# Performance work log

Hardware: AMD Instinct MI355X
Metric: run time of the kernel (lower is better)

Reference implementation:

```python
import jax, jax.numpy as jnp
import numpy as np

W_WORKERS = 2
Q_LEN = 16
HIDDEN = 4096
N_HEADS = 32
N_KV = 8
HEAD_DIM = 128
L_SHARED = 8192
L_WORKER = 2048
THETA = 10000.0


def rotate_half(x):
    x1, x2 = jnp.split(x, 2, axis=-1)
    return jnp.concatenate((-x2, x1), axis=-1)


def rope_cos_sin(pos):
    # pos: int array [...]; returns cos,sin of shape [..., HEAD_DIM] (HF convention: freqs duplicated)
    inv = 1.0 / (THETA ** (jnp.arange(0, HEAD_DIM, 2, dtype=jnp.float32) / HEAD_DIM))
    ang = pos[..., None].astype(jnp.float32) * inv
    emb = jnp.concatenate((ang, ang), axis=-1)
    return jnp.cos(emb), jnp.sin(emb)


def setup_inputs() -> dict:
    key = jax.random.key(0)
    ks = jax.random.split(key, 16)
    std = 0.02
    # new keys are appended at positions L_WORKER..L_WORKER+Q-1 of each worker's own segment
    pos_new = jnp.broadcast_to(L_WORKER + jnp.arange(Q_LEN), (W_WORKERS, Q_LEN))
    cos_new, sin_new = rope_cos_sin(pos_new)
    return {
        'hidden_states': jax.random.normal(ks[0], (W_WORKERS, Q_LEN, HIDDEN), jnp.float32),
        'Wq': jax.random.normal(ks[1], (N_HEADS * HEAD_DIM, HIDDEN), jnp.float32) * std,
        'bq': jnp.zeros((N_HEADS * HEAD_DIM,), jnp.float32),
        'Wk': jax.random.normal(ks[2], (N_KV * HEAD_DIM, HIDDEN), jnp.float32) * std,
        'bk': jnp.zeros((N_KV * HEAD_DIM,), jnp.float32),
        'Wv': jax.random.normal(ks[3], (N_KV * HEAD_DIM, HIDDEN), jnp.float32) * std,
        'bv': jnp.zeros((N_KV * HEAD_DIM,), jnp.float32),
        'Wo': jax.random.normal(ks[4], (HIDDEN, N_HEADS * HEAD_DIM), jnp.float32) * std,
        'seg_shared_k': jax.random.normal(ks[5], (N_KV, L_SHARED, HEAD_DIM), jnp.float32),
        'seg_shared_v': jax.random.normal(ks[6], (N_KV, L_SHARED, HEAD_DIM), jnp.float32),
        'w0_k': jax.random.normal(ks[7], (N_KV, L_WORKER, HEAD_DIM), jnp.float32),
        'w0_v': jax.random.normal(ks[8], (N_KV, L_WORKER, HEAD_DIM), jnp.float32),
        'w1_k': jax.random.normal(ks[9], (N_KV, L_WORKER, HEAD_DIM), jnp.float32),
        'w1_v': jax.random.normal(ks[10], (N_KV, L_WORKER, HEAD_DIM), jnp.float32),
        'cos_new': cos_new,
        'sin_new': sin_new,
    }


def reference(hidden_states, Wq, bq, Wk, bk, Wv, bv, Wo,
              seg_shared_k, seg_shared_v, w0_k, w0_v, w1_k, w1_v,
              cos_new, sin_new):
    W, Q, _ = hidden_states.shape
    scale = HEAD_DIM ** -0.5
    # projections -> [W, n_heads, Q, D]
    q = (hidden_states @ Wq.T + bq).reshape(W, Q, N_HEADS, HEAD_DIM).transpose(0, 2, 1, 3)
    k_new = (hidden_states @ Wk.T + bk).reshape(W, Q, N_KV, HEAD_DIM).transpose(0, 2, 1, 3)
    v_new = (hidden_states @ Wv.T + bv).reshape(W, Q, N_KV, HEAD_DIM).transpose(0, 2, 1, 3)
    # rope new keys (unsqueeze_dim=1: broadcast over kv heads)
    c, s = cos_new[:, None], sin_new[:, None]
    k_new = k_new * c + rotate_half(k_new) * s
    # cache update: segment 0 = shared prompt, segment 1/2 = worker 0/1 own cache (grows by Q)
    keys = [seg_shared_k,
            jnp.concatenate([w0_k, k_new[0]], axis=1),
            jnp.concatenate([w1_k, k_new[1]], axis=1)]
    values = [seg_shared_v,
              jnp.concatenate([w0_v, v_new[0]], axis=1),
              jnp.concatenate([w1_v, v_new[1]], axis=1)]
    frag_lens = [L_SHARED, L_WORKER + Q, L_WORKER + Q]
    # worker w's view: [shared, other worker's cache, own cache]
    orders = [[0, 2, 1], [0, 1, 2]]
    loc = np.zeros((3, W_WORKERS, Q), dtype=np.int32)
    for w, order in enumerate(orders):
        pos = 0
        for seg in reversed(order):
            pos += frag_lens[seg]
            loc[seg, w] = np.arange(pos - Q, pos)
    loc = jnp.asarray(loc)  # [S, W, Q]
    cos_q, sin_q = rope_cos_sin(loc)  # [S, W, Q, D]
    # hogwild_rope: queries rotated per (segment, worker) location -> [S, W, H, Q, D]
    rq = q[None] * cos_q[:, :, None] + rotate_half(q)[None] * sin_q[:, :, None]
    rep = N_HEADS // N_KV
    scores, v_parts = [], []
    for seg in range(3):
        k_s = jnp.repeat(keys[seg], rep, axis=0)  # GQA expand [H, L_s, D]
        sc = jnp.einsum('whqd,hld->whql', rq[seg], k_s) * scale
        mask = jnp.arange(frag_lens[seg])[None, None, None, :] <= loc[seg][:, None, :, None]
        scores.append(jnp.where(mask, sc, jnp.finfo(sc.dtype).min))
        v_parts.append(jnp.repeat(values[seg], rep, axis=0))
    scores = jnp.concatenate(scores, axis=-1)        # [W, H, Q, Ltot] joint softmax over fragments
    probs = jax.nn.softmax(scores, axis=-1)
    v_all = jnp.concatenate(v_parts, axis=1)         # [H, Ltot, D]
    attn = jnp.einsum('whql,hld->whqd', probs, v_all)
    out = attn.transpose(0, 2, 1, 3).reshape(W, Q, N_HEADS * HEAD_DIM) @ Wo.T
    return out
```

## Files before the change

### kernel.cpp

```cpp
#include <hip/hip_runtime.h>
#include <hip/hip_fp16.h>
#include <cstdint>
#include <cstddef>

#define QL 16
#define LSH 8192
#define LWK 2048
#define SCALE 0.08838834764831845f

typedef __attribute__((ext_vector_type(8))) short short8;
typedef __attribute__((ext_vector_type(4))) short short4v;
typedef __attribute__((ext_vector_type(4))) float f32x4;
typedef __attribute__((ext_vector_type(8))) unsigned short ushort8v;

#if defined(__has_builtin)
#if __has_builtin(__builtin_amdgcn_mfma_f32_16x16x16bf16_1k)
#define HAVE_MFMA16 1
#endif
#endif

__device__ __forceinline__ unsigned short f2bf(float f) {
  unsigned int u = __float_as_uint(f);
  u += 0x7fffu + ((u >> 16) & 1u);
  return (unsigned short)(u >> 16);
}
__device__ __forceinline__ float bf2f(unsigned short b) {
  return __uint_as_float(((unsigned int)b) << 16);
}

__device__ __forceinline__ void gload_lds16(const float* g, float* lds) {
  __builtin_amdgcn_global_load_lds(
      (const __attribute__((address_space(1))) void*)g,
      (__attribute__((address_space(3))) void*)lds, 16, 0, 0);
}

__device__ __forceinline__ void gload_f4(float4& d, const float* p) {
  asm volatile("global_load_dwordx4 %0, %1, off"
               : "=v"(d)
               : "v"((const __attribute__((address_space(1))) float*)p));
}
__device__ __forceinline__ void gload_f1(float& d, const float* p) {
  asm volatile("global_load_dword %0, %1, off"
               : "=v"(d)
               : "v"((const __attribute__((address_space(1))) float*)p));
}
__device__ __forceinline__ void gload_s8(short8& d, const unsigned short* p) {
  asm volatile("global_load_dwordx4 %0, %1, off"
               : "=v"(d)
               : "v"((const __attribute__((address_space(1))) unsigned short*)p));
}

__global__ __launch_bounds__(256) void k_cast(
    const float* __restrict__ in, unsigned short* __restrict__ outp, int n4)
{
  int i = blockIdx.x * 256 + threadIdx.x;
  if (i < n4) {
    float4 v = ((const float4*)in)[i];
    ushort4 p; p.x = f2bf(v.x); p.y = f2bf(v.y); p.z = f2bf(v.z); p.w = f2bf(v.w);
    ((ushort4*)outp)[i] = p;
  }
}

__global__ __launch_bounds__(256) void k_gemm4(
    const unsigned short* __restrict__ Xbf,
    const float* __restrict__ W0, const float* __restrict__ W1, const float* __restrict__ W2,
    const float* __restrict__ b0, const float* __restrict__ b1, const float* __restrict__ b2,
    float* __restrict__ outA, float* __restrict__ outB, int Ntot)
{
  __shared__ float Ws[2][16 * 516];
  const int bx = blockIdx.x;
  const int n0 = (bx >> 1) * 16;
  const int khalf = bx & 1;
  const float* W; const float* bias; int row0;
  if (n0 < 4096)      { W = W0; bias = b0; row0 = n0; }
  else if (n0 < 5120) { W = W1; bias = b1; row0 = n0 - 4096; }
  else                { W = W2; bias = b2; row0 = n0 - 5120; }
  const int t = threadIdx.x;
  const int w_id = t >> 6;
  const int lane = t & 63;
  const int l15 = lane & 15;
  const int quad = lane >> 4;
  const int cb0 = khalf * 2048;
  const int wk = w_id * 128;

  f32x4 C0 = {0.f,0.f,0.f,0.f}, C1 = {0.f,0.f,0.f,0.f};
  short8 xa0[4], xa1[4];

  auto stage = [&](int c, int b) {
    const int cbase = cb0 + c * 512;
#pragma unroll
    for (int i = 0; i < 8; ++i) {
      int idx = w_id * 8 + i;
      int r = idx >> 1, hh = idx & 1;
      const float* g = W + (size_t)(row0 + r) * 4096 + cbase + hh * 256 + lane * 4;
      gload_lds16(g, &Ws[b][r * 516 + hh * 256]);
    }
  };

  stage(0, 0);
#pragma unroll
  for (int c = 0; c < 4; ++c) {
    const int cbase = cb0 + c * 512;
#pragma unroll
    for (int ks = 0; ks < 4; ++ks) {
      int ko = wk + ks * 32 + quad * 8;
      gload_s8(xa0[ks], Xbf + (size_t)l15 * 4096 + cbase + ko);
      gload_s8(xa1[ks], Xbf + (size_t)(16 + l15) * 4096 + cbase + ko);
    }
    __builtin_amdgcn_sched_barrier(0);
    if (c < 3) {
      stage(c + 1, (c + 1) & 1);
      asm volatile("s_waitcnt vmcnt(8)" ::: "memory");
    } else {
      asm volatile("s_waitcnt vmcnt(0)" ::: "memory");
    }
    __builtin_amdgcn_sched_barrier(0);
    __builtin_amdgcn_s_barrier();
    __builtin_amdgcn_sched_barrier(0);
    const float* Wsb = Ws[c & 1];
#pragma unroll
    for (int ks = 0; ks < 4; ++ks) {
      int ko = wk + ks * 32 + quad * 8;
      f32x4 wlo = *(const f32x4*)(&Wsb[l15 * 516 + ko]);
      f32x4 whi = *(const f32x4*)(&Wsb[l15 * 516 + ko + 4]);
      short8 bfr;
      bfr[0] = (short)f2bf(wlo[0]); bfr[1] = (short)f2bf(wlo[1]);
      bfr[2] = (short)f2bf(wlo[2]); bfr[3] = (short)f2bf(wlo[3]);
      bfr[4] = (short)f2bf(whi[0]); bfr[5] = (short)f2bf(whi[1]);
      bfr[6] = (short)f2bf(whi[2]); bfr[7] = (short)f2bf(whi[3]);
      C0 = __builtin_amdgcn_mfma_f32_16x16x32_bf16(xa0[ks], bfr, C0, 0, 0, 0);
      C1 = __builtin_amdgcn_mfma_f32_16x16x32_bf16(xa1[ks], bfr, C1, 0, 0, 0);
    }
    __builtin_amdgcn_sched_barrier(0);
    __builtin_amdgcn_s_barrier();
    __builtin_amdgcn_sched_barrier(0);
  }
  float* Red = &Ws[0][0];
#pragma unroll
  for (int i = 0; i < 4; ++i) {
    Red[w_id * 512 + (quad * 4 + i) * 16 + l15] = C0[i];
    Red[w_id * 512 + 256 + (quad * 4 + i) * 16 + l15] = C1[i];
  }
  __syncthreads();
  float* dst = khalf ? outB : outA;
#pragma unroll
  for (int e = t; e < 512; e += 256) {
    float s = Red[e] + Red[512 + e] + Red[1024 + e] + Red[1536 + e];
    int m = e >> 4, n = e & 15;
    if (khalf == 0 && bias) s += bias[row0 + n];
    dst[(size_t)m * Ntot + n0 + n] = s;
  }
}

__global__ __launch_bounds__(256) void k_add(
    const float* __restrict__ A, const float* __restrict__ B,
    float* __restrict__ o, int n4)
{
  int i = blockIdx.x * 256 + threadIdx.x;
  if (i < n4) {
    float4 a = ((const float4*)A)[i], b = ((const float4*)B)[i];
    float4 r; r.x = a.x + b.x; r.y = a.y + b.y; r.z = a.z + b.z; r.w = a.w + b.w;
    ((float4*)o)[i] = r;
  }
}

__global__ __launch_bounds__(256) void k_rope(
    const float* __restrict__ qA, const float* __restrict__ qB,
    const float* __restrict__ cosn, const float* __restrict__ sinn,
    unsigned short* __restrict__ rq, unsigned short* __restrict__ knew,
    unsigned short* __restrict__ vnew)
{
  const int g = blockIdx.x * 256 + threadIdx.x;
  const float LOGTH = 9.210340371976184f;
  if (g < 393216) {
    int d = g & 127, q = (g >> 7) & 15, head = (g >> 11) & 31, w = (g >> 16) & 1, var = g >> 17;
    int tok = w * 16 + q;
    int col = head * 128 + d;
    size_t ix = (size_t)tok * 6144 + col;
    float val = qA[ix] + qB[ix];
    size_t ir = (d < 64) ? ix + 64 : ix - 64;
    float rot = qA[ir] + qB[ir];
    if (d < 64) rot = -rot;
    int pos = (var == 0 ? 12304 : (var == 1 ? 4112 : 2048)) + q;
    int i = d & 63;
    float inv = expf(-(float)i * (LOGTH / 64.0f));
    float ang = (float)pos * inv;
    float c = cosf(ang), s = sinf(ang);
    rq[g] = f2bf((val * c + rot * s) * SCALE);
  } else {
    int g2 = g - 393216;
    if (g2 < 65536) {
      int isv = (g2 >= 32768);
      if (isv) g2 -= 32768;
      int d = g2 & 127, q = (g2 >> 7) & 15, h = (g2 >> 11) & 7, w = (g2 >> 14) & 1;
      int tok = w * 16 + q;
      if (isv) {
        size_t ix = (size_t)tok * 6144 + 5120 + h * 128 + d;
        vnew[g2] = f2bf(qA[ix] + qB[ix]);
      } else {
        size_t ix = (size_t)tok * 6144 + 4096 + h * 128 + d;
        float val = qA[ix] + qB[ix];
        size_t ir = (d < 64) ? ix + 64 : ix - 64;
        float rot = qA[ir] + qB[ir];
        if (d < 64) rot = -rot;
        float c = cosn[tok * 128 + d], s = sinn[tok * 128 + d];
        knew[g2] = f2bf(val * c + rot * s);
      }
    }
  }
}

__global__ __launch_bounds__(512, 2) void k_attn(
    const float* __restrict__ shk, const float* __restrict__ shv,
    const float* __restrict__ w0k, const float* __restrict__ w0v,
    const float* __restrict__ w1k, const float* __restrict__ w1v,
    const unsigned short* __restrict__ rq,
    const unsigned short* __restrict__ knew, const unsigned short* __restrict__ vnew,
    __half* __restrict__ accP, float* __restrict__ lP)
{
  __shared__ alignas(16) unsigned short Ks[2][64 * 136];
  __shared__ alignas(16) unsigned short Vts[2][128 * 72];
#ifndef HAVE_MFMA16
  __shared__ alignas(16) unsigned short Plds[8 * 16 * 72];
#endif

  const int h = blockIdx.x / 50;
  const int cidx = blockIdx.x % 50;
  int kind, k0, nk; bool is_new;
  if (cidx < 32)      { kind = 0; k0 = cidx * 256; nk = 256; is_new = false; }
  else if (cidx < 41) { int c = cidx - 32; kind = 1; k0 = c * 256; nk = (c == 8) ? 16 : 256; is_new = (c == 8); }
  else                { int c = cidx - 41; kind = 2; k0 = c * 256; nk = (c == 8) ? 16 : 256; is_new = (c == 8); }

  const int t = threadIdx.x;
  const int w_id = t >> 6;
  const int lane = t & 63;
  const int l15 = lane & 15;
  const int quad = lane >> 4;
  const int worker = w_id >> 2;
  const int hq = w_id & 3;
  const int col4 = t & 31;
  const int rowb = t >> 5;
  const int dv = t & 127;
  const int tg = t >> 7;

  int var; bool causal;
  if (kind == 0)      { var = 0; causal = false; }
  else if (kind == 1) { var = (worker == 0) ? 2 : 1; causal = (worker == 0); }
  else                { var = (worker == 1) ? 2 : 1; causal = (worker == 1); }

  const float* Ksrc = (kind == 0) ? (shk + (size_t)h * LSH * 128)
                     : (kind == 1) ? (w0k + (size_t)h * LWK * 128)
                                   : (w1k + (size_t)h * LWK * 128);
  const float* Vsrc = (kind == 0) ? (shv + (size_t)h * LSH * 128)
                     : (kind == 1) ? (w0v + (size_t)h * LWK * 128)
                                   : (w1v + (size_t)h * LWK * 128);
  const int wseg = (kind == 2) ? 1 : 0;
  const unsigned short* knsrc = knew + ((size_t)wseg * 8 + h) * 16 * 128;
  const unsigned short* vnsrc = vnew + ((size_t)wseg * 8 + h) * 16 * 128;

  const int head = h * 4 + hq;
  short8 arq[4];
  {
    const unsigned short* base =
        rq + ((((size_t)var * 2 + worker) * 32 + head) * 16 + l15) * 128 + quad * 8;
#pragma unroll
    for (int ks = 0; ks < 4; ++ks) arq[ks] = *(const short8*)(base + ks * 32);
  }

  float lrow = 0.f;
  f32x4 acc[8];
#pragma unroll
  for (int dt = 0; dt < 8; ++dt) acc[dt] = {0.f,0.f,0.f,0.f};

  float4 kf[4];
  float  vf[16];

  const float* kbase = Ksrc + (size_t)(k0 + rowb) * 128 + col4 * 4;
  const float* vbase = Vsrc + (size_t)(k0 + tg * 8) * 128 + dv;

  auto issue_tile = [&](int st) {
    const float* kp = kbase + (size_t)st * 64 * 128;
#pragma unroll
    for (int i = 0; i < 4; ++i) gload_f4(kf[i], kp + (size_t)i * 16 * 128);
    const float* vp = vbase + (size_t)st * 64 * 128;
#pragma unroll
    for (int g = 0; g < 2; ++g)
#pragma unroll
      for (int i = 0; i < 8; ++i)
        gload_f1(vf[g * 8 + i], vp + (size_t)(g * 32 + i) * 128);
  };

  const int nst = (nk + 63) >> 6;
  if (!is_new) {
    issue_tile(0);
  } else {
#pragma unroll
    for (int i = 0; i < 4; ++i) {
      ushort4 p = *(const ushort4*)(knsrc + (size_t)((i * 16 + rowb) & 15) * 128 + col4 * 4);
      kf[i].x = bf2f(p.x); kf[i].y = bf2f(p.y);
      kf[i].z = bf2f(p.z); kf[i].w = bf2f(p.w);
    }
#pragma unroll
    for (int g = 0; g < 2; ++g)
#pragma unroll
      for (int i = 0; i < 8; ++i)
        vf[g * 8 + i] = bf2f(vnsrc[(size_t)((g * 32 + tg * 8 + i) & 15) * 128 + dv]);
  }

  for (int st = 0; st < nst; ++st) {
    const int pb = st & 1;
    asm volatile("s_waitcnt vmcnt(0)" ::: "memory");
    __builtin_amdgcn_sched_barrier(0);
#pragma unroll
    for (int i = 0; i < 4; ++i) {
      ushort4 p; p.x = f2bf(kf[i].x); p.y = f2bf(kf[i].y);
      p.z = f2bf(kf[i].z); p.w = f2bf(kf[i].w);
      *(ushort4*)(&Ks[pb][(i * 16 + rowb) * 136 + col4 * 4]) = p;
    }
#pragma unroll
    for (int g = 0; g < 2; ++g) {
      ushort8v p;
#pragma unroll
      for (int i = 0; i < 8; ++i) p[i] = f2bf(vf[g * 8 + i]);
      *(ushort8v*)(&Vts[pb][dv * 72 + (g * 4 + tg) * 8]) = p;
    }
    if (st + 1 < nst) issue_tile(st + 1);
    asm volatile("s_waitcnt lgkmcnt(0)" ::: "memory");
    __builtin_amdgcn_sched_barrier(0);
    __builtin_amdgcn_s_barrier();
    __builtin_amdgcn_sched_barrier(0);

    f32x4 S[4];
#pragma unroll
    for (int nt = 0; nt < 4; ++nt) S[nt] = {0.f,0.f,0.f,0.f};
#pragma unroll
    for (int ks = 0; ks < 4; ++ks)
#pragma unroll
      for (int nt = 0; nt < 4; ++nt) {
        short8 kfr = *(const short8*)(&Ks[pb][(nt * 16 + l15) * 136 + ks * 32 + quad * 8]);
        S[nt] = __builtin_amdgcn_mfma_f32_16x16x32_bf16(kfr, arq[ks], S[nt], 0, 0, 0);
      }
    if (is_new) {
#pragma unroll
      for (int nt = 0; nt < 4; ++nt)
#pragma unroll
        for (int i = 0; i < 4; ++i) {
          int loc = st * 64 + nt * 16 + quad * 4 + i;
          if (loc >= nk || (causal && loc > l15)) S[nt][i] = -3.0e38f;
        }
    }
    float rs = 0.0f;
#pragma unroll
    for (int nt = 0; nt < 4; ++nt)
#pragma unroll
      for (int i = 0; i < 4; ++i) {
        float p = __expf(fminf(S[nt][i], 60.0f));
        S[nt][i] = p;
        rs += p;
      }
#ifdef HAVE_MFMA16
    short4v pv[4];
#pragma unroll
    for (int nt = 0; nt < 4; ++nt) {
      short4v pp;
      pp[0] = (short)f2bf(S[nt][0]); pp[1] = (short)f2bf(S[nt][1]);
      pp[2] = (short)f2bf(S[nt][2]); pp[3] = (short)f2bf(S[nt][3]);
      pv[nt] = pp;
    }
#else
#pragma unroll
    for (int nt = 0; nt < 4; ++nt)
#pragma unroll
      for (int i = 0; i < 4; ++i)
        Plds[w_id * (16 * 72) + l15 * 72 + nt * 16 + quad * 4 + i] = f2bf(S[nt][i]);
#endif
    rs += __shfl_xor(rs, 16, 64);
    rs += __shfl_xor(rs, 32, 64);
    lrow += rs;

#ifdef HAVE_MFMA16
#pragma unroll
    for (int dt = 0; dt < 8; ++dt)
#pragma unroll
      for (int kc = 0; kc < 4; ++kc) {
        short4v vfr = *(const short4v*)(&Vts[pb][(dt * 16 + l15) * 72 + kc * 16 + quad * 4]);
        acc[dt] = __builtin_amdgcn_mfma_f32_16x16x16bf16_1k(pv[kc], vfr, acc[dt], 0, 0, 0);
      }
#else
    short8 ap[2];
#pragma unroll
    for (int ks2 = 0; ks2 < 2; ++ks2)
      ap[ks2] = *(const short8*)(
          &Plds[w_id * (16 * 72) + l15 * 72 + ks2 * 32 + quad * 8]);
#pragma unroll
    for (int dt = 0; dt < 8; ++dt)
#pragma unroll
      for (int ks2 = 0; ks2 < 2; ++ks2) {
        short8 vfr = *(const short8*)(&Vts[pb][(dt * 16 + l15) * 72 + ks2 * 32 + quad * 8]);
        acc[dt] = __builtin_amdgcn_mfma_f32_16x16x32_bf16(ap[ks2], vfr, acc[dt], 0, 0, 0);
      }
#endif
  }

  __half* accB = accP + (size_t)blockIdx.x * 128 * 128;
  const int wrow = worker * 64 + hq * 16;
#pragma unroll
  for (int dt = 0; dt < 8; ++dt)
#pragma unroll
    for (int i = 0; i < 4; ++i) {
      int row = wrow + quad * 4 + i;
      int d = dt * 16 + l15;
      accB[row * 128 + d] = __float2half(acc[dt][i]);
    }
  if (quad == 0) {
    int row = wrow + l15;
    lP[(size_t)blockIdx.x * 128 + row] = lrow;
  }
}

__global__ __launch_bounds__(128) void k_combine(
    const __half* __restrict__ accP, const float* __restrict__ lP,
    unsigned short* __restrict__ attnX)
{
  __shared__ float sl[50];
  const int h = blockIdx.x >> 7;
  const int r = blockIdx.x & 127;
  const int d = threadIdx.x;
  if (d < 50) sl[d] = lP[(size_t)(h * 50 + d) * 128 + r];
  __syncthreads();
  float L = 0.0f, A = 0.0f;
#pragma unroll
  for (int c = 0; c < 50; ++c) L += sl[c];
#pragma unroll
  for (int cc = 0; cc < 50; cc += 10) {
    float p[10];
#pragma unroll
    for (int i = 0; i < 10; ++i)
      p[i] = __half2float(accP[((size_t)(h * 50 + cc + i) * 128 + r) * 128 + d]);
#pragma unroll
    for (int i = 0; i < 10; ++i) A += p[i];
  }
  int workerv = r >> 6, headpairv = (r >> 5) & 1, mtv = (r >> 4) & 1, q = r & 15;
  int head = h * 4 + headpairv * 2 + mtv;
  attnX[(size_t)(workerv * 16 + q) * 4096 + head * 128 + d] = f2bf(A / L);
}

extern "C" void kernel_launch(void* const* d_in, const int* in_sizes, int n_in,
                              void* d_out, int out_size, void* d_ws, size_t ws_size,
                              hipStream_t stream)
{
  const float* hs   = (const float*)d_in[0];
  const float* Wq   = (const float*)d_in[1];
  const float* bq   = (const float*)d_in[2];
  const float* Wk   = (const float*)d_in[3];
  const float* bk   = (const float*)d_in[4];
  const float* Wv   = (const float*)d_in[5];
  const float* bv   = (const float*)d_in[6];
  const float* Wo   = (const float*)d_in[7];
  const float* shk  = (const float*)d_in[8];
  const float* shv  = (const float*)d_in[9];
  const float* w0k  = (const float*)d_in[10];
  const float* w0v  = (const float*)d_in[11];
  const float* w1k  = (const float*)d_in[12];
  const float* w1v  = (const float*)d_in[13];
  const float* cosn = (const float*)d_in[14];
  const float* sinn = (const float*)d_in[15];
  float* out = (float*)d_out;

  char* ws = (char*)d_ws;
  float*          qkvA   = (float*)(ws + 0);
  unsigned short* rq     = (unsigned short*)(ws + 786432);
  unsigned short* knew   = (unsigned short*)(ws + 1572864);
  unsigned short* vnew   = (unsigned short*)(ws + 1638400);
  unsigned short* hsbf   = (unsigned short*)(ws + 1703936);
  unsigned short* attnXb = (unsigned short*)(ws + 1966080);
  float*          lP     = (float*)(ws + 2228224);
  __half*         accP   = (__half*)(ws + 2433024);
  float*          qkvB   = (float*)(ws + 15540224);
  float*          outA   = (float*)(ws + 2433024);
  float*          outB   = (float*)(ws + 2433024 + 786432);

  k_cast<<<128, 256, 0, stream>>>(hs, hsbf, 32768);
  k_gemm4<<<768, 256, 0, stream>>>(hsbf, Wq, Wk, Wv, bq, bk, bv, qkvA, qkvB, 6144);
  k_rope<<<1792, 256, 0, stream>>>(qkvA, qkvB, cosn, sinn, rq, knew, vnew);
  k_attn<<<400, 512, 0, stream>>>(shk, shv, w0k, w0v, w1k, w1v, rq, knew, vnew, accP, lP);
  k_combine<<<1024, 128, 0, stream>>>(accP, lP, attnXb);
  k_gemm4<<<512, 256, 0, stream>>>(attnXb, Wo, Wo, Wo, nullptr, nullptr, nullptr, outA, outB, 4096);
  k_add<<<192, 256, 0, stream>>>(outA, outB, out, 49152);
}
```

Before: 295.4 us.

## Split GEMMs four ways along K and halve attention chunk size for more blocks

Both projection GEMMs now split the K dimension into four partial products instead of two, doubling block count and adding launch bound occupancy hints. The partial sums are combined in the rope and add kernels. The attention kernel now uses 128-key chunks (98 per head group instead of 50), with a single LDS buffer and two sequential stages, and the combine kernel reduces over more partials. The aim is to fill more compute units on a small decode-size workload, at the cost of more partial-result traffic and reduction work. The k_add launch also shrinks from 49152 to 32768 float4 elements, which now matches the 32x4096 output.

```diff
diff --git a/kernel.cpp b/kernel.cpp
--- a/kernel.cpp
+++ b/kernel.cpp
@@ -61,16 +61,17 @@
   }
 }
 
-__global__ __launch_bounds__(256) void k_gemm4(
+__global__ __launch_bounds__(256, 2) void k_gemm4(
     const unsigned short* __restrict__ Xbf,
     const float* __restrict__ W0, const float* __restrict__ W1, const float* __restrict__ W2,
     const float* __restrict__ b0, const float* __restrict__ b1, const float* __restrict__ b2,
-    float* __restrict__ outA, float* __restrict__ outB, int Ntot)
+    float* __restrict__ outA, float* __restrict__ outB,
+    float* __restrict__ outC, float* __restrict__ outD, int Ntot)
 {
   __shared__ float Ws[2][16 * 516];
   const int bx = blockIdx.x;
-  const int n0 = (bx >> 1) * 16;
-  const int khalf = bx & 1;
+  const int n0 = (bx >> 2) * 16;
+  const int kq = bx & 3;
   const float* W; const float* bias; int row0;
   if (n0 < 4096)      { W = W0; bias = b0; row0 = n0; }
   else if (n0 < 5120) { W = W1; bias = b1; row0 = n0 - 4096; }
@@ -80,44 +81,38 @@
   const int lane = t & 63;
   const int l15 = lane & 15;
   const int quad = lane >> 4;
-  const int cb0 = khalf * 2048;
+  const int cb0 = kq * 1024;
   const int wk = w_id * 128;
 
   f32x4 C0 = {0.f,0.f,0.f,0.f}, C1 = {0.f,0.f,0.f,0.f};
-  short8 xa0[4], xa1[4];
-
-  auto stage = [&](int c, int b) {
+  short8 xa0[2][4], xa1[2][4];
+
+#pragma unroll
+  for (int c = 0; c < 2; ++c) {
     const int cbase = cb0 + c * 512;
 #pragma unroll
     for (int i = 0; i < 8; ++i) {
       int idx = w_id * 8 + i;
       int r = idx >> 1, hh = idx & 1;
       const float* g = W + (size_t)(row0 + r) * 4096 + cbase + hh * 256 + lane * 4;
-      gload_lds16(g, &Ws[b][r * 516 + hh * 256]);
-    }
-  };
-
-  stage(0, 0);
-#pragma unroll
-  for (int c = 0; c < 4; ++c) {
-    const int cbase = cb0 + c * 512;
+      gload_lds16(g, &Ws[c][r * 516 + hh * 256]);
+    }
 #pragma unroll
     for (int ks = 0; ks < 4; ++ks) {
       int ko = wk + ks * 32 + quad * 8;
-      gload_s8(xa0[ks], Xbf + (size_t)l15 * 4096 + cbase + ko);
-      gload_s8(xa1[ks], Xbf + (size_t)(16 + l15) * 4096 + cbase + ko);
-    }
-    __builtin_amdgcn_sched_barrier(0);
-    if (c < 3) {
-      stage(c + 1, (c + 1) & 1);
-      asm volatile("s_waitcnt vmcnt(8)" ::: "memory");
-    } else {
-      asm volatile("s_waitcnt vmcnt(0)" ::: "memory");
-    }
+      gload_s8(xa0[c][ks], Xbf + (size_t)l15 * 4096 + cbase + ko);
+      gload_s8(xa1[c][ks], Xbf + (size_t)(16 + l15) * 4096 + cbase + ko);
+    }
+  }
+  __builtin_amdgcn_sched_barrier(0);
+#pragma unroll
+  for (int c = 0; c < 2; ++c) {
+    if (c == 0) asm volatile("s_waitcnt vmcnt(16)" ::: "memory");
+    else        asm volatile("s_waitcnt vmcnt(0)"  ::: "memory");
     __builtin_amdgcn_sched_barrier(0);
     __builtin_amdgcn_s_barrier();
     __builtin_amdgcn_sched_barrier(0);
-    const float* Wsb = Ws[c & 1];
+    const float* Wsb = Ws[c];
 #pragma unroll
     for (int ks = 0; ks < 4; ++ks) {
       int ko = wk + ks * 32 + quad * 8;
@@ -128,12 +123,9 @@
       bfr[2] = (short)f2bf(wlo[2]); bfr[3] = (short)f2bf(wlo[3]);
       bfr[4] = (short)f2bf(whi[0]); bfr[5] = (short)f2bf(whi[1]);
       bfr[6] = (short)f2bf(whi[2]); bfr[7] = (short)f2bf(whi[3]);
-      C0 = __builtin_amdgcn_mfma_f32_16x16x32_bf16(xa0[ks], bfr, C0, 0, 0, 0);
-      C1 = __builtin_amdgcn_mfma_f32_16x16x32_bf16(xa1[ks], bfr, C1, 0, 0, 0);
-    }
-    __builtin_amdgcn_sched_barrier(0);
-    __builtin_amdgcn_s_barrier();
-    __builtin_amdgcn_sched_barrier(0);
+      C0 = __builtin_amdgcn_mfma_f32_16x16x32_bf16(xa0[c][ks], bfr, C0, 0, 0, 0);
+      C1 = __builtin_amdgcn_mfma_f32_16x16x32_bf16(xa1[c][ks], bfr, C1, 0, 0, 0);
+    }
   }
   float* Red = &Ws[0][0];
 #pragma unroll
@@ -142,30 +134,35 @@
     Red[w_id * 512 + 256 + (quad * 4 + i) * 16 + l15] = C1[i];
   }
   __syncthreads();
-  float* dst = khalf ? outB : outA;
+  float* dst = (kq == 0) ? outA : (kq == 1) ? outB : (kq == 2) ? outC : outD;
 #pragma unroll
   for (int e = t; e < 512; e += 256) {
     float s = Red[e] + Red[512 + e] + Red[1024 + e] + Red[1536 + e];
     int m = e >> 4, n = e & 15;
-    if (khalf == 0 && bias) s += bias[row0 + n];
+    if (kq == 0 && bias) s += bias[row0 + n];
     dst[(size_t)m * Ntot + n0 + n] = s;
   }
 }
 
 __global__ __launch_bounds__(256) void k_add(
     const float* __restrict__ A, const float* __restrict__ B,
+    const float* __restrict__ C, const float* __restrict__ D,
     float* __restrict__ o, int n4)
 {
   int i = blockIdx.x * 256 + threadIdx.x;
   if (i < n4) {
     float4 a = ((const float4*)A)[i], b = ((const float4*)B)[i];
-    float4 r; r.x = a.x + b.x; r.y = a.y + b.y; r.z = a.z + b.z; r.w = a.w + b.w;
+    float4 c = ((const float4*)C)[i], d = ((const float4*)D)[i];
+    float4 r;
+    r.x = (a.x + b.x) + (c.x + d.x); r.y = (a.y + b.y) + (c.y + d.y);
+    r.z = (a.z + b.z) + (c.z + d.z); r.w = (a.w + b.w) + (c.w + d.w);
     ((float4*)o)[i] = r;
   }
 }
 
 __global__ __launch_bounds__(256) void k_rope(
     const float* __restrict__ qA, const float* __restrict__ qB,
+    const float* __restrict__ qC, const float* __restrict__ qD,
     const float* __restrict__ cosn, const float* __restrict__ sinn,
     unsigned short* __restrict__ rq, unsigned short* __restrict__ knew,
     unsigned short* __restrict__ vnew)
@@ -177,9 +174,9 @@
     int tok = w * 16 + q;
     int col = head * 128 + d;
     size_t ix = (size_t)tok * 6144 + col;
-    float val = qA[ix] + qB[ix];
+    float val = (qA[ix] + qB[ix]) + (qC[ix] + qD[ix]);
     size_t ir = (d < 64) ? ix + 64 : ix - 64;
-    float rot = qA[ir] + qB[ir];
+    float rot = (qA[ir] + qB[ir]) + (qC[ir] + qD[ir]);
     if (d < 64) rot = -rot;
     int pos = (var == 0 ? 12304 : (var == 1 ? 4112 : 2048)) + q;
     int i = d & 63;
@@ -196,12 +193,12 @@
       int tok = w * 16 + q;
       if (isv) {
         size_t ix = (size_t)tok * 6144 + 5120 + h * 128 + d;
-        vnew[g2] = f2bf(qA[ix] + qB[ix]);
+        vnew[g2] = f2bf((qA[ix] + qB[ix]) + (qC[ix] + qD[ix]));
       } else {
         size_t ix = (size_t)tok * 6144 + 4096 + h * 128 + d;
-        float val = qA[ix] + qB[ix];
+        float val = (qA[ix] + qB[ix]) + (qC[ix] + qD[ix]);
         size_t ir = (d < 64) ? ix + 64 : ix - 64;
-        float rot = qA[ir] + qB[ir];
+        float rot = (qA[ir] + qB[ir]) + (qC[ir] + qD[ir]);
         if (d < 64) rot = -rot;
         float c = cosn[tok * 128 + d], s = sinn[tok * 128 + d];
         knew[g2] = f2bf(val * c + rot * s);
@@ -218,18 +215,18 @@
     const unsigned short* __restrict__ knew, const unsigned short* __restrict__ vnew,
     __half* __restrict__ accP, float* __restrict__ lP)
 {
-  __shared__ alignas(16) unsigned short Ks[2][64 * 136];
-  __shared__ alignas(16) unsigned short Vts[2][128 * 72];
+  __shared__ alignas(16) unsigned short Ks[64 * 136];
+  __shared__ alignas(16) unsigned short Vts[128 * 72];
 #ifndef HAVE_MFMA16
   __shared__ alignas(16) unsigned short Plds[8 * 16 * 72];
 #endif
 
-  const int h = blockIdx.x / 50;
-  const int cidx = blockIdx.x % 50;
+  const int h = blockIdx.x / 98;
+  const int cidx = blockIdx.x % 98;
   int kind, k0, nk; bool is_new;
-  if (cidx < 32)      { kind = 0; k0 = cidx * 256; nk = 256; is_new = false; }
-  else if (cidx < 41) { int c = cidx - 32; kind = 1; k0 = c * 256; nk = (c == 8) ? 16 : 256; is_new = (c == 8); }
-  else                { int c = cidx - 41; kind = 2; k0 = c * 256; nk = (c == 8) ? 16 : 256; is_new = (c == 8); }
+  if (cidx < 64)      { kind = 0; k0 = cidx * 128; nk = 128; is_new = false; }
+  else if (cidx < 81) { int c = cidx - 64; kind = 1; k0 = c * 128; nk = (c == 16) ? 16 : 128; is_new = (c == 16); }
+  else                { int c = cidx - 81; kind = 2; k0 = c * 128; nk = (c == 16) ? 16 : 128; is_new = (c == 16); }
 
   const int t = threadIdx.x;
   const int w_id = t >> 6;
@@ -290,46 +287,23 @@
         gload_f1(vf[g * 8 + i], vp + (size_t)(g * 32 + i) * 128);
   };
 
-  const int nst = (nk + 63) >> 6;
-  if (!is_new) {
-    issue_tile(0);
-  } else {
-#pragma unroll
-    for (int i = 0; i < 4; ++i) {
-      ushort4 p = *(const ushort4*)(knsrc + (size_t)((i * 16 + rowb) & 15) * 128 + col4 * 4);
-      kf[i].x = bf2f(p.x); kf[i].y = bf2f(p.y);
-      kf[i].z = bf2f(p.z); kf[i].w = bf2f(p.w);
-    }
-#pragma unroll
-    for (int g = 0; g < 2; ++g)
-#pragma unroll
-      for (int i = 0; i < 8; ++i)
-        vf[g * 8 + i] = bf2f(vnsrc[(size_t)((g * 32 + tg * 8 + i) & 15) * 128 + dv]);
-  }
-
-  for (int st = 0; st < nst; ++st) {
-    const int pb = st & 1;
-    asm volatile("s_waitcnt vmcnt(0)" ::: "memory");
-    __builtin_amdgcn_sched_barrier(0);
+  auto lds_write = [&]() {
 #pragma unroll
     for (int i = 0; i < 4; ++i) {
       ushort4 p; p.x = f2bf(kf[i].x); p.y = f2bf(kf[i].y);
       p.z = f2bf(kf[i].z); p.w = f2bf(kf[i].w);
-      *(ushort4*)(&Ks[pb][(i * 16 + rowb) * 136 + col4 * 4]) = p;
+      *(ushort4*)(&Ks[(i * 16 + rowb) * 136 + col4 * 4]) = p;
     }
 #pragma unroll
     for (int g = 0; g < 2; ++g) {
       ushort8v p;
 #pragma unroll
       for (int i = 0; i < 8; ++i) p[i] = f2bf(vf[g * 8 + i]);
-      *(ushort8v*)(&Vts[pb][dv * 72 + (g * 4 + tg) * 8]) = p;
-    }
-    if (st + 1 < nst) issue_tile(st + 1);
-    asm volatile("s_waitcnt lgkmcnt(0)" ::: "memory");
-    __builtin_amdgcn_sched_barrier(0);
-    __builtin_amdgcn_s_barrier();
-    __builtin_amdgcn_sched_barrier(0);
-
+      *(ushort8v*)(&Vts[dv * 72 + (g * 4 + tg) * 8]) = p;
+    }
+  };
+
+  auto compute = [&](int st) {
     f32x4 S[4];
 #pragma unroll
     for (int nt = 0; nt < 4; ++nt) S[nt] = {0.f,0.f,0.f,0.f};
@@ -337,7 +311,7 @@
     for (int ks = 0; ks < 4; ++ks)
 #pragma unroll
       for (int nt = 0; nt < 4; ++nt) {
-        short8 kfr = *(const short8*)(&Ks[pb][(nt * 16 + l15) * 136 + ks * 32 + quad * 8]);
+        short8 kfr = *(const short8*)(&Ks[(nt * 16 + l15) * 136 + ks * 32 + quad * 8]);
         S[nt] = __builtin_amdgcn_mfma_f32_16x16x32_bf16(kfr, arq[ks], S[nt], 0, 0, 0);
       }
     if (is_new) {
@@ -383,7 +357,7 @@
     for (int dt = 0; dt < 8; ++dt)
 #pragma unroll
       for (int kc = 0; kc < 4; ++kc) {
-        short4v vfr = *(const short4v*)(&Vts[pb][(dt * 16 + l15) * 72 + kc * 16 + quad * 4]);
+        short4v vfr = *(const short4v*)(&Vts[(dt * 16 + l15) * 72 + kc * 16 + quad * 4]);
         acc[dt] = __builtin_amdgcn_mfma_f32_16x16x16bf16_1k(pv[kc], vfr, acc[dt], 0, 0, 0);
       }
 #else
@@ -396,10 +370,49 @@
     for (int dt = 0; dt < 8; ++dt)
 #pragma unroll
       for (int ks2 = 0; ks2 < 2; ++ks2) {
-        short8 vfr = *(const short8*)(&Vts[pb][(dt * 16 + l15) * 72 + ks2 * 32 + quad * 8]);
+        short8 vfr = *(const short8*)(&Vts[(dt * 16 + l15) * 72 + ks2 * 32 + quad * 8]);
         acc[dt] = __builtin_amdgcn_mfma_f32_16x16x32_bf16(ap[ks2], vfr, acc[dt], 0, 0, 0);
       }
 #endif
+  };
+
+  const int nst = (nk == 16) ? 1 : 2;
+  if (!is_new) {
+    issue_tile(0);
+  } else {
+#pragma unroll
+    for (int i = 0; i < 4; ++i) {
+      ushort4 p = *(const ushort4*)(knsrc + (size_t)((i * 16 + rowb) & 15) * 128 + col4 * 4);
+      kf[i].x = bf2f(p.x); kf[i].y = bf2f(p.y);
+      kf[i].z = bf2f(p.z); kf[i].w = bf2f(p.w);
+    }
+#pragma unroll
+    for (int g = 0; g < 2; ++g)
+#pragma unroll
+      for (int i = 0; i < 8; ++i)
+        vf[g * 8 + i] = bf2f(vnsrc[(size_t)((g * 32 + tg * 8 + i) & 15) * 128 + dv]);
+  }
+
+  asm volatile("s_waitcnt vmcnt(0)" ::: "memory");
+  __builtin_amdgcn_sched_barrier(0);
+  lds_write();
+  if (nst > 1) issue_tile(1);
+  asm volatile("s_waitcnt lgkmcnt(0)" ::: "memory");
+  __builtin_amdgcn_sched_barrier(0);
+  __builtin_amdgcn_s_barrier();
+  __builtin_amdgcn_sched_barrier(0);
+  compute(0);
+
+  if (nst > 1) {
+    __syncthreads();
+    asm volatile("s_waitcnt vmcnt(0)" ::: "memory");
+    __builtin_amdgcn_sched_barrier(0);
+    lds_write();
+    asm volatile("s_waitcnt lgkmcnt(0)" ::: "memory");
+    __builtin_amdgcn_sched_barrier(0);
+    __builtin_amdgcn_s_barrier();
+    __builtin_amdgcn_sched_barrier(0);
+    compute(1);
   }
 
   __half* accB = accP + (size_t)blockIdx.x * 128 * 128;
@@ -422,26 +435,26 @@
     const __half* __restrict__ accP, const float* __restrict__ lP,
     unsigned short* __restrict__ attnX)
 {
-  __shared__ float sl[50];
+  __shared__ float sl[98];
   const int h = blockIdx.x >> 7;
   const int r = blockIdx.x & 127;
   const int d = threadIdx.x;
-  if (d < 50) sl[d] = lP[(size_t)(h * 50 + d) * 128 + r];
+  if (d < 98) sl[d] = lP[(size_t)(h * 98 + d) * 128 + r];
   __syncthreads();
   float L = 0.0f, A = 0.0f;
 #pragma unroll
-  for (int c = 0; c < 50; ++c) L += sl[c];
-#pragma unroll
-  for (int cc = 0; cc < 50; cc += 10) {
-    float p[10];
-#pragma unroll
-    for (int i = 0; i < 10; ++i)
-      p[i] = __half2float(accP[((size_t)(h * 50 + cc + i) * 128 + r) * 128 + d]);
-#pragma unroll
-    for (int i = 0; i < 10; ++i) A += p[i];
-  }
-  int workerv = r >> 6, headpairv = (r >> 5) & 1, mtv = (r >> 4) & 1, q = r & 15;
-  int head = h * 4 + headpairv * 2 + mtv;
+  for (int c = 0; c < 98; ++c) L += sl[c];
+#pragma unroll
+  for (int cc = 0; cc < 98; cc += 7) {
+    float p[7];
+#pragma unroll
+    for (int i = 0; i < 7; ++i)
+      p[i] = __half2float(accP[((size_t)(h * 98 + cc + i) * 128 + r) * 128 + d]);
+#pragma unroll
+    for (int i = 0; i < 7; ++i) A += p[i];
+  }
+  int workerv = r >> 6, hqv = (r >> 4) & 3, q = r & 15;
+  int head = h * 4 + hqv;
   attnX[(size_t)(workerv * 16 + q) * 4096 + head * 128 + d] = f2bf(A / L);
 }
 
@@ -468,23 +481,29 @@
   float* out = (float*)d_out;
 
   char* ws = (char*)d_ws;
-  float*          qkvA   = (float*)(ws + 0);
-  unsigned short* rq     = (unsigned short*)(ws + 786432);
-  unsigned short* knew   = (unsigned short*)(ws + 1572864);
-  unsigned short* vnew   = (unsigned short*)(ws + 1638400);
-  unsigned short* hsbf   = (unsigned short*)(ws + 1703936);
-  unsigned short* attnXb = (unsigned short*)(ws + 1966080);
-  float*          lP     = (float*)(ws + 2228224);
-  __half*         accP   = (__half*)(ws + 2433024);
-  float*          qkvB   = (float*)(ws + 15540224);
-  float*          outA   = (float*)(ws + 2433024);
-  float*          outB   = (float*)(ws + 2433024 + 786432);
+  unsigned short* rq     = (unsigned short*)(ws + 0);
+  unsigned short* knew   = (unsigned short*)(ws + 786432);
+  unsigned short* vnew   = (unsigned short*)(ws + 851968);
+  unsigned short* hsbf   = (unsigned short*)(ws + 917504);
+  unsigned short* attnXb = (unsigned short*)(ws + 1179648);
+  float*          lP     = (float*)(ws + 1441792);
+  __half*         accP   = (__half*)(ws + 1843200);
+  float*          qkvA   = (float*)(ws + 1843200);
+  float*          qkvB   = (float*)(ws + 1843200 + 786432);
+  float*          qkvC   = (float*)(ws + 1843200 + 2 * 786432);
+  float*          qkvD   = (float*)(ws + 1843200 + 3 * 786432);
+  float*          outA   = (float*)(ws + 1843200);
+  float*          outB   = (float*)(ws + 1843200 + 524288);
+  float*          outC   = (float*)(ws + 1843200 + 2 * 524288);
+  float*          outD   = (float*)(ws + 1843200 + 3 * 524288);
 
   k_cast<<<128, 256, 0, stream>>>(hs, hsbf, 32768);
-  k_gemm4<<<768, 256, 0, stream>>>(hsbf, Wq, Wk, Wv, bq, bk, bv, qkvA, qkvB, 6144);
-  k_rope<<<1792, 256, 0, stream>>>(qkvA, qkvB, cosn, sinn, rq, knew, vnew);
-  k_attn<<<400, 512, 0, stream>>>(shk, shv, w0k, w0v, w1k, w1v, rq, knew, vnew, accP, lP);
+  k_gemm4<<<1536, 256, 0, stream>>>(hsbf, Wq, Wk, Wv, bq, bk, bv,
+                                    qkvA, qkvB, qkvC, qkvD, 6144);
+  k_rope<<<1792, 256, 0, stream>>>(qkvA, qkvB, qkvC, qkvD, cosn, sinn, rq, knew, vnew);
+  k_attn<<<784, 512, 0, stream>>>(shk, shv, w0k, w0v, w1k, w1v, rq, knew, vnew, accP, lP);
   k_combine<<<1024, 128, 0, stream>>>(accP, lP, attnXb);
-  k_gemm4<<<512, 256, 0, stream>>>(attnXb, Wo, Wo, Wo, nullptr, nullptr, nullptr, outA, outB, 4096);
-  k_add<<<192, 256, 0, stream>>>(outA, outB, out, 49152);
-}
+  k_gemm4<<<1024, 256, 0, stream>>>(attnXb, Wo, Wo, Wo, nullptr, nullptr, nullptr,
+                                    outA, outB, outC, outD, 4096);
+  k_add<<<128, 256, 0, stream>>>(outA, outB, outC, outD, out, 32768);
+}
```

New measurement: 296.1 us. Within noise of the previous version (+0.3%).
